# Performance work log

Measured on AMD Instinct MI355X. Metric: run time of the kernel, lower is better.

## Reference

```python
import jax, jax.numpy as jnp
import numpy as np

B, H, S, D = 2, 16, 2048, 64

def setup_inputs() -> dict:
    key = jax.random.key(0)
    kq, kk, kv, km, ks = jax.random.split(key, 5)
    return {
        "query_input": jax.random.normal(kq, (B, H, S, D), dtype=jnp.float32),
        "key_input": jax.random.normal(kk, (B, H, S, D), dtype=jnp.float32),
        "value_input": jax.random.normal(kv, (B, H, S, D), dtype=jnp.float32),
        "query_mask": jnp.ones((B, 1, S, 1), dtype=jnp.float32),
        "key_mask": jax.random.uniform(km, (B, 1, 1, S), dtype=jnp.float32),
        "scale_factor": jax.random.normal(ks, (B, 1, 1, 1), dtype=jnp.float32),
        "dropout": 0,
    }

def reference(query_input, key_input, value_input, query_mask, key_mask, scale_factor, dropout):
    # qk = q @ k^T  -> [B, H, S, S]
    qk = jnp.einsum("bhqd,bhkd->bhqk", query_input, key_input)
    scaled_qk = qk * scale_factor                      # elementwise per-batch scale
    softmax_qk = jax.nn.softmax(scaled_qk, axis=-1)
    masked = softmax_qk * key_mask                     # post-softmax multiplicative mask
    # dropout with p=0 is the identity (deterministic baseline)
    output = jnp.einsum("bhqk,bhkd->bhqd", masked, value_input)
    return output
```

## Files before the change

kernel.cpp:

```cpp
#include <hip/hip_runtime.h>
#include <hip/hip_bf16.h>
#include <stdint.h>

#define BB 2
#define HH 16
#define SS 2048
#define DD 64
constexpr int BH = BB * HH;
constexpr int NT = SS / 64;
constexpr int QB = 16;

typedef _Float16 f16_t;
typedef f16_t f16x8 __attribute__((ext_vector_type(8)));
typedef float f32x4 __attribute__((ext_vector_type(4)));

__device__ __forceinline__ uint32_t pkf16(float a, float b) {
    return __builtin_bit_cast(uint32_t, __builtin_amdgcn_cvt_pkrtz(a, b));
}
__device__ __forceinline__ float fmax3(float a, float b, float c) {
    return fmaxf(fmaxf(a, b), c);
}

__global__ __launch_bounds__(256)
void prepack(const float* __restrict__ Kg, const float* __restrict__ Vg,
             const float* __restrict__ Mg, f16_t* __restrict__ Kp,
             f16_t* __restrict__ Vp)
{
    __shared__ float Vs[64][65];
    const int bh = blockIdx.x % BH;
    const int kt = blockIdx.x / BH;
    const int b  = bh / HH;
    const int t  = threadIdx.x;
    const size_t gbase = (size_t)bh * SS * DD + (size_t)kt * 64 * DD;
    const size_t tbase = ((size_t)bh * NT + kt) * 4096;

    for (int c = t; c < 512; c += 256) {
        const int row = c >> 3, j = c & 7;
        const float* kp = Kg + gbase + (size_t)row * DD + j * 8;
        float4 a = *(const float4*)kp;
        float4 d = *(const float4*)(kp + 4);
        uint4 w = make_uint4(pkf16(a.x, a.y), pkf16(a.z, a.w),
                             pkf16(d.x, d.y), pkf16(d.z, d.w));
        *(uint4*)&Kp[tbase + (size_t)row * 64 + ((j ^ (row & 7)) * 8)] = w;
    }

    for (int c = t; c < 1024; c += 256) {
        const int key = c >> 4, dc = (c & 15) * 4;
        float4 v = *(const float4*)(Vg + gbase + (size_t)key * DD + dc);
        const float m = Mg[(size_t)b * SS + kt * 64 + key];
        Vs[key][dc + 0] = v.x * m;
        Vs[key][dc + 1] = v.y * m;
        Vs[key][dc + 2] = v.z * m;
        Vs[key][dc + 3] = v.w * m;
    }
    __syncthreads();

    for (int c = t; c < 512; c += 256) {
        const int dr = c >> 3, j = c & 7;
        float v0 = Vs[j * 8 + 0][dr], v1 = Vs[j * 8 + 1][dr];
        float v2 = Vs[j * 8 + 2][dr], v3 = Vs[j * 8 + 3][dr];
        float v4 = Vs[j * 8 + 4][dr], v5 = Vs[j * 8 + 5][dr];
        float v6 = Vs[j * 8 + 6][dr], v7 = Vs[j * 8 + 7][dr];
        uint4 w = make_uint4(pkf16(v0, v1), pkf16(v2, v3),
                             pkf16(v4, v5), pkf16(v6, v7));
        *(uint4*)&Vp[tbase + (size_t)dr * 64 + ((j ^ (dr & 7)) * 8)] = w;
    }
}

__global__ __launch_bounds__(512)
void fattn10(const float* __restrict__ Qg, const f16_t* __restrict__ Kp,
             const f16_t* __restrict__ Vp, const float* __restrict__ Sg,
             float* __restrict__ Og)
{
    __shared__ __align__(16) f16_t Kt[2][4096];
    __shared__ __align__(16) f16_t Vt[3][4096];
    __shared__ __align__(16) f16_t Pt[8][16][72];

    const int bh   = blockIdx.x % BH;
    const int qt   = blockIdx.x / BH;
    const int b    = bh / HH;
    const int tid  = threadIdx.x;
    const int wave = tid >> 6;
    const int lane = tid & 63;
    const int l16  = lane & 15;
    const int quad = lane >> 4;

    const float sc = Sg[b] * 1.44269504088896340736f;
    const size_t base = (size_t)bh * SS * DD;
    const size_t tb0  = (size_t)bh * NT * 4096;
    const int q0 = qt * 128 + wave * 16;

    auto stage = [&](int kt, int kbuf, int vbuf) {
        const f16_t* ks = Kp + tb0 + (size_t)kt * 4096 + tid * 8;
        const f16_t* vs = Vp + tb0 + (size_t)kt * 4096 + tid * 8;
        __builtin_amdgcn_global_load_lds(
            (const __attribute__((address_space(1))) void*)ks,
            (__attribute__((address_space(3))) void*)&Kt[kbuf][wave * 512],
            16, 0, 0);
        __builtin_amdgcn_global_load_lds(
            (const __attribute__((address_space(1))) void*)vs,
            (__attribute__((address_space(3))) void*)&Vt[vbuf][wave * 512],
            16, 0, 0);
    };

    stage(0, 0, 0);

    f16x8 qf[2];
    {
        const float* qp = Qg + base + (size_t)(q0 + l16) * DD + quad * 8;
#pragma unroll
        for (int kc = 0; kc < 2; ++kc) {
            float4 a  = *(const float4*)(qp + kc * 32);
            float4 b4 = *(const float4*)(qp + kc * 32 + 4);
            f16x8 f;
            f[0] = (f16_t)(a.x * sc);  f[1] = (f16_t)(a.y * sc);
            f[2] = (f16_t)(a.z * sc);  f[3] = (f16_t)(a.w * sc);
            f[4] = (f16_t)(b4.x * sc); f[5] = (f16_t)(b4.y * sc);
            f[6] = (f16_t)(b4.z * sc); f[7] = (f16_t)(b4.w * sc);
            qf[kc] = f;
        }
    }

    f16x8 ones;
#pragma unroll
    for (int i = 0; i < 8; ++i) ones[i] = (f16_t)1.0f;

    f32x4 Ot[4];
#pragma unroll
    for (int mt = 0; mt < 4; ++mt) Ot[mt] = f32x4{0.f, 0.f, 0.f, 0.f};
    f32x4 Osum = f32x4{0.f, 0.f, 0.f, 0.f};
    float m_run = -1e30f;

    const int swz = (l16 & 7) << 3;

    int vcur = 0;
    for (int kt = 0; kt < NT; ++kt) {
        const int kcur = kt & 1;
        const int vnxt = (vcur == 2) ? 0 : vcur + 1;
        if (kt + 1 < NT) {
            stage(kt + 1, kcur ^ 1, vnxt);
            asm volatile("s_waitcnt vmcnt(2)" ::: "memory");
        } else {
            asm volatile("s_waitcnt vmcnt(0)" ::: "memory");
        }
        __builtin_amdgcn_s_barrier();

        __builtin_amdgcn_s_setprio(1);
        f32x4 Sfr[4];
#pragma unroll
        for (int mt = 0; mt < 4; ++mt) {
            f32x4 acc = f32x4{0.f, 0.f, 0.f, 0.f};
#pragma unroll
            for (int kc = 0; kc < 2; ++kc) {
                const int off = (mt * 16 + l16) * 64 + ((kc * 32 + quad * 8) ^ swz);
                f16x8 kh = *(const f16x8*)&Kt[kcur][off];
                acc = __builtin_amdgcn_mfma_f32_16x16x32_f16(kh, qf[kc], acc, 0, 0, 0);
            }
            Sfr[mt] = acc;
        }

        if (kt > 0) {
            const int vprv = (vcur == 0) ? 2 : vcur - 1;
#pragma unroll
            for (int kc = 0; kc < 2; ++kc) {
                f16x8 pf = *(const f16x8*)&Pt[wave][l16][kc * 32 + quad * 8];
#pragma unroll
                for (int mt = 0; mt < 4; ++mt) {
                    const int off = (mt * 16 + l16) * 64 + ((kc * 32 + quad * 8) ^ swz);
                    f16x8 vf = *(const f16x8*)&Vt[vprv][off];
                    Ot[mt] = __builtin_amdgcn_mfma_f32_16x16x32_f16(vf, pf, Ot[mt], 0, 0, 0);
                }
                Osum = __builtin_amdgcn_mfma_f32_16x16x32_f16(ones, pf, Osum, 0, 0, 0);
            }
        }
        __builtin_amdgcn_s_setprio(0);

        float g0 = fmax3(Sfr[0][0], Sfr[0][1], Sfr[0][2]);
        float g1 = fmax3(Sfr[0][3], Sfr[1][0], Sfr[1][1]);
        float g2 = fmax3(Sfr[1][2], Sfr[1][3], Sfr[2][0]);
        float g3 = fmax3(Sfr[2][1], Sfr[2][2], Sfr[2][3]);
        float g4 = fmax3(Sfr[3][0], Sfr[3][1], Sfr[3][2]);
        float h0 = fmax3(g0, g1, Sfr[3][3]);
        float h1 = fmax3(g2, g3, g4);
        const float lmax = fmaxf(h0, h1);

        if (__any(lmax > m_run + 8.0f)) {
            float mxq = fmaxf(lmax, __shfl_xor(lmax, 16));
            mxq = fmaxf(mxq, __shfl_xor(mxq, 32));
            const float mnew  = fmaxf(m_run, mxq);
            const float alpha = __builtin_amdgcn_exp2f(m_run - mnew);
            m_run = mnew;
#pragma unroll
            for (int mt = 0; mt < 4; ++mt) Ot[mt] *= alpha;
            Osum *= alpha;
        }

        float ps[4][4];
#pragma unroll
        for (int mt = 0; mt < 4; ++mt)
#pragma unroll
            for (int r = 0; r < 4; ++r)
                ps[mt][r] = __builtin_amdgcn_exp2f(Sfr[mt][r] - m_run);

#pragma unroll
        for (int mt = 0; mt < 4; ++mt) {
            uint2 w = make_uint2(pkf16(ps[mt][0], ps[mt][1]),
                                 pkf16(ps[mt][2], ps[mt][3]));
            *(uint2*)&Pt[wave][l16][mt * 16 + quad * 4] = w;
        }

        __builtin_amdgcn_s_barrier();
        vcur = vnxt;
    }

    {
        const int vprv = (vcur == 0) ? 2 : vcur - 1;
#pragma unroll
        for (int kc = 0; kc < 2; ++kc) {
            f16x8 pf = *(const f16x8*)&Pt[wave][l16][kc * 32 + quad * 8];
#pragma unroll
            for (int mt = 0; mt < 4; ++mt) {
                const int off = (mt * 16 + l16) * 64 + ((kc * 32 + quad * 8) ^ swz);
                f16x8 vf = *(const f16x8*)&Vt[vprv][off];
                Ot[mt] = __builtin_amdgcn_mfma_f32_16x16x32_f16(vf, pf, Ot[mt], 0, 0, 0);
            }
            Osum = __builtin_amdgcn_mfma_f32_16x16x32_f16(ones, pf, Osum, 0, 0, 0);
        }
    }

    const float inv = 1.0f / Osum[0];
    float* op = Og + base + (size_t)(q0 + l16) * DD + quad * 4;
#pragma unroll
    for (int mt = 0; mt < 4; ++mt) {
#pragma unroll
        for (int r = 0; r < 4; ++r)
            op[mt * 16 + r] = Ot[mt][r] * inv;
    }
}

__global__ __launch_bounds__(512)
void fattn6(const float* __restrict__ Qg, const float* __restrict__ Kg,
            const float* __restrict__ Vg, const float* __restrict__ Mg,
            const float* __restrict__ Sg, float* __restrict__ Og)
{
    __shared__ __align__(16) f16_t Kh_lds[64][72];
    __shared__ __align__(16) f16_t Vt_lds[64][72];
    __shared__ __align__(16) f16_t Pt_lds[8][16][72];
    __shared__ float msk_lds[SS];

    const int bh   = blockIdx.x % BH;
    const int qt   = blockIdx.x / BH;
    const int b    = bh / HH;
    const int tid  = threadIdx.x;
    const int wave = tid >> 6;
    const int lane = tid & 63;
    const int l16  = lane & 15;
    const int quad = lane >> 4;

    const float sc = Sg[b] * 1.44269504088896340736f;
    const size_t base = (size_t)bh * SS * DD;
    const int q0 = qt * 128 + wave * 16;

    for (int i = tid; i < SS; i += 512) msk_lds[i] = Mg[(size_t)b * SS + i];

    f16x8 qf[2];
    {
        const float* qp = Qg + base + (size_t)(q0 + l16) * DD + quad * 8;
#pragma unroll
        for (int kc = 0; kc < 2; ++kc) {
            float4 a  = *(const float4*)(qp + kc * 32);
            float4 b4 = *(const float4*)(qp + kc * 32 + 4);
            f16x8 f;
            f[0] = (f16_t)(a.x * sc);  f[1] = (f16_t)(a.y * sc);
            f[2] = (f16_t)(a.z * sc);  f[3] = (f16_t)(a.w * sc);
            f[4] = (f16_t)(b4.x * sc); f[5] = (f16_t)(b4.y * sc);
            f[6] = (f16_t)(b4.z * sc); f[7] = (f16_t)(b4.w * sc);
            qf[kc] = f;
        }
    }

    f32x4 Ot[4];
#pragma unroll
    for (int mt = 0; mt < 4; ++mt) Ot[mt] = f32x4{0.f, 0.f, 0.f, 0.f};
    float m_run = -1e30f, l_run = 0.0f;

    const int krow = tid >> 3;
    const int kc8  = (tid & 7) * 8;
    const int vd   = tid & 63;
    const int vk0  = (tid >> 6) * 8;

    for (int kt = 0; kt < NT; ++kt) {
        __syncthreads();
        {
            const float* kp = Kg + base + (size_t)(kt * 64 + krow) * DD + kc8;
            float4 a0 = *(const float4*)(kp);
            float4 a1 = *(const float4*)(kp + 4);
            uint4 w = make_uint4(pkf16(a0.x, a0.y), pkf16(a0.z, a0.w),
                                 pkf16(a1.x, a1.y), pkf16(a1.z, a1.w));
            *(uint4*)&Kh_lds[krow][kc8] = w;
        }
        {
            const float* vp = Vg + base + (size_t)(kt * 64 + vk0) * DD + vd;
            const float* mp = &msk_lds[kt * 64 + vk0];
            float v0 = vp[0 * DD] * mp[0], v1 = vp[1 * DD] * mp[1];
            float v2 = vp[2 * DD] * mp[2], v3 = vp[3 * DD] * mp[3];
            float v4 = vp[4 * DD] * mp[4], v5 = vp[5 * DD] * mp[5];
            float v6 = vp[6 * DD] * mp[6], v7 = vp[7 * DD] * mp[7];
            uint4 w = make_uint4(pkf16(v0, v1), pkf16(v2, v3),
                                 pkf16(v4, v5), pkf16(v6, v7));
            *(uint4*)&Vt_lds[vd][vk0] = w;
        }
        __syncthreads();

        f32x4 Sfr[4];
#pragma unroll
        for (int mt = 0; mt < 4; ++mt) {
            f32x4 acc = f32x4{0.f, 0.f, 0.f, 0.f};
#pragma unroll
            for (int kc = 0; kc < 2; ++kc) {
                f16x8 kh = *(const f16x8*)&Kh_lds[mt * 16 + l16][kc * 32 + quad * 8];
                acc = __builtin_amdgcn_mfma_f32_16x16x32_f16(kh, qf[kc], acc, 0, 0, 0);
            }
            Sfr[mt] = acc;
        }

        float mx = Sfr[0][0];
#pragma unroll
        for (int mt = 0; mt < 4; ++mt)
#pragma unroll
            for (int r = 0; r < 4; ++r) mx = fmaxf(mx, Sfr[mt][r]);
        mx = fmaxf(mx, __shfl_xor(mx, 16));
        mx = fmaxf(mx, __shfl_xor(mx, 32));

        if (__any(mx > m_run)) {
            const float mnew  = fmaxf(m_run, mx);
            const float alpha = exp2f(m_run - mnew);
            m_run = mnew;
            l_run *= alpha;
#pragma unroll
            for (int mt = 0; mt < 4; ++mt) Ot[mt] *= alpha;
        }

        float ps[4][4];
        float rs = 0.0f;
#pragma unroll
        for (int mt = 0; mt < 4; ++mt)
#pragma unroll
            for (int r = 0; r < 4; ++r) {
                ps[mt][r] = exp2f(Sfr[mt][r] - m_run);
                rs += ps[mt][r];
            }
        rs += __shfl_xor(rs, 16);
        rs += __shfl_xor(rs, 32);
        l_run += rs;

#pragma unroll
        for (int mt = 0; mt < 4; ++mt) {
            uint2 w = make_uint2(pkf16(ps[mt][0], ps[mt][1]),
                                 pkf16(ps[mt][2], ps[mt][3]));
            *(uint2*)&Pt_lds[wave][l16][mt * 16 + quad * 4] = w;
        }

#pragma unroll
        for (int kc = 0; kc < 2; ++kc) {
            f16x8 pf = *(const f16x8*)&Pt_lds[wave][l16][kc * 32 + quad * 8];
#pragma unroll
            for (int mt = 0; mt < 4; ++mt) {
                f16x8 vf = *(const f16x8*)&Vt_lds[mt * 16 + l16][kc * 32 + quad * 8];
                Ot[mt] = __builtin_amdgcn_mfma_f32_16x16x32_f16(vf, pf, Ot[mt], 0, 0, 0);
            }
        }
    }

    const float inv = 1.0f / l_run;
    float* op = Og + base + (size_t)(q0 + l16) * DD + quad * 4;
#pragma unroll
    for (int mt = 0; mt < 4; ++mt) {
#pragma unroll
        for (int r = 0; r < 4; ++r)
            op[mt * 16 + r] = Ot[mt][r] * inv;
    }
}

extern "C" void kernel_launch(void* const* d_in, const int* in_sizes, int n_in,
                              void* d_out, int out_size, void* d_ws, size_t ws_size,
                              hipStream_t stream) {
    const float* Qg = (const float*)d_in[0];
    const float* Kg = (const float*)d_in[1];
    const float* Vg = (const float*)d_in[2];
    const float* Mg = (const float*)d_in[4];
    const float* Sg = (const float*)d_in[5];
    float* Og = (float*)d_out;

    const size_t kv_elems = (size_t)BH * SS * DD;
    const size_t need = 2 * kv_elems * sizeof(f16_t);

    if (d_ws != nullptr && ws_size >= need) {
        f16_t* Kp = (f16_t*)d_ws;
        f16_t* Vp = Kp + kv_elems;
        prepack<<<dim3(BH * NT), dim3(256), 0, stream>>>(Kg, Vg, Mg, Kp, Vp);
        fattn10<<<dim3(BH * QB), dim3(512), 0, stream>>>(Qg, Kp, Vp, Sg, Og);
    } else {
        fattn6<<<dim3(BH * QB), dim3(512), 0, stream>>>(Qg, Kg, Vg, Mg, Sg, Og);
    }
}
```

Before: 146.6 us.

## Give each wave two 16-row query groups to reuse K/V fragments

```diff
diff --git a/kernel.cpp b/kernel.cpp
--- a/kernel.cpp
+++ b/kernel.cpp
@@ -67,14 +67,14 @@
     }
 }
 
-__global__ __launch_bounds__(512)
-void fattn10(const float* __restrict__ Qg, const f16_t* __restrict__ Kp,
+__global__ __launch_bounds__(256)
+void fattn12(const float* __restrict__ Qg, const f16_t* __restrict__ Kp,
              const f16_t* __restrict__ Vp, const float* __restrict__ Sg,
              float* __restrict__ Og)
 {
     __shared__ __align__(16) f16_t Kt[2][4096];
     __shared__ __align__(16) f16_t Vt[3][4096];
-    __shared__ __align__(16) f16_t Pt[8][16][72];
+    __shared__ __align__(16) f16_t Pt[4][2][16][72];
 
     const int bh   = blockIdx.x % BH;
     const int qt   = blockIdx.x / BH;
@@ -88,26 +88,36 @@
     const float sc = Sg[b] * 1.44269504088896340736f;
     const size_t base = (size_t)bh * SS * DD;
     const size_t tb0  = (size_t)bh * NT * 4096;
-    const int q0 = qt * 128 + wave * 16;
+    const int q0 = qt * 128 + wave * 32;
 
     auto stage = [&](int kt, int kbuf, int vbuf) {
-        const f16_t* ks = Kp + tb0 + (size_t)kt * 4096 + tid * 8;
-        const f16_t* vs = Vp + tb0 + (size_t)kt * 4096 + tid * 8;
+        const size_t toff = tb0 + (size_t)kt * 4096 + wave * 1024 + lane * 8;
+        const f16_t* ks = Kp + toff;
+        const f16_t* vs = Vp + toff;
         __builtin_amdgcn_global_load_lds(
             (const __attribute__((address_space(1))) void*)ks,
-            (__attribute__((address_space(3))) void*)&Kt[kbuf][wave * 512],
+            (__attribute__((address_space(3))) void*)&Kt[kbuf][wave * 1024],
+            16, 0, 0);
+        __builtin_amdgcn_global_load_lds(
+            (const __attribute__((address_space(1))) void*)(ks + 512),
+            (__attribute__((address_space(3))) void*)&Kt[kbuf][wave * 1024 + 512],
             16, 0, 0);
         __builtin_amdgcn_global_load_lds(
             (const __attribute__((address_space(1))) void*)vs,
-            (__attribute__((address_space(3))) void*)&Vt[vbuf][wave * 512],
+            (__attribute__((address_space(3))) void*)&Vt[vbuf][wave * 1024],
+            16, 0, 0);
+        __builtin_amdgcn_global_load_lds(
+            (const __attribute__((address_space(1))) void*)(vs + 512),
+            (__attribute__((address_space(3))) void*)&Vt[vbuf][wave * 1024 + 512],
             16, 0, 0);
     };
 
     stage(0, 0, 0);
 
-    f16x8 qf[2];
-    {
-        const float* qp = Qg + base + (size_t)(q0 + l16) * DD + quad * 8;
+    f16x8 qf[2][2];
+#pragma unroll
+    for (int g = 0; g < 2; ++g) {
+        const float* qp = Qg + base + (size_t)(q0 + g * 16 + l16) * DD + quad * 8;
 #pragma unroll
         for (int kc = 0; kc < 2; ++kc) {
             float4 a  = *(const float4*)(qp + kc * 32);
@@ -117,7 +127,7 @@
             f[2] = (f16_t)(a.z * sc);  f[3] = (f16_t)(a.w * sc);
             f[4] = (f16_t)(b4.x * sc); f[5] = (f16_t)(b4.y * sc);
             f[6] = (f16_t)(b4.z * sc); f[7] = (f16_t)(b4.w * sc);
-            qf[kc] = f;
+            qf[g][kc] = f;
         }
     }
 
@@ -125,11 +135,13 @@
 #pragma unroll
     for (int i = 0; i < 8; ++i) ones[i] = (f16_t)1.0f;
 
-    f32x4 Ot[4];
-#pragma unroll
-    for (int mt = 0; mt < 4; ++mt) Ot[mt] = f32x4{0.f, 0.f, 0.f, 0.f};
-    f32x4 Osum = f32x4{0.f, 0.f, 0.f, 0.f};
-    float m_run = -1e30f;
+    f32x4 Ot[2][4];
+#pragma unroll
+    for (int g = 0; g < 2; ++g)
+#pragma unroll
+        for (int mt = 0; mt < 4; ++mt) Ot[g][mt] = f32x4{0.f, 0.f, 0.f, 0.f};
+    f32x4 Osum[2] = {f32x4{0.f, 0.f, 0.f, 0.f}, f32x4{0.f, 0.f, 0.f, 0.f}};
+    float m_run[2] = {-1e30f, -1e30f};
 
     const int swz = (l16 & 7) << 3;
 
@@ -139,74 +151,83 @@
         const int vnxt = (vcur == 2) ? 0 : vcur + 1;
         if (kt + 1 < NT) {
             stage(kt + 1, kcur ^ 1, vnxt);
-            asm volatile("s_waitcnt vmcnt(2)" ::: "memory");
+            asm volatile("s_waitcnt vmcnt(4)" ::: "memory");
         } else {
             asm volatile("s_waitcnt vmcnt(0)" ::: "memory");
         }
         __builtin_amdgcn_s_barrier();
 
         __builtin_amdgcn_s_setprio(1);
-        f32x4 Sfr[4];
+        f32x4 Sfr[2][4];
 #pragma unroll
         for (int mt = 0; mt < 4; ++mt) {
-            f32x4 acc = f32x4{0.f, 0.f, 0.f, 0.f};
+            f32x4 a0 = f32x4{0.f, 0.f, 0.f, 0.f};
+            f32x4 a1 = f32x4{0.f, 0.f, 0.f, 0.f};
 #pragma unroll
             for (int kc = 0; kc < 2; ++kc) {
                 const int off = (mt * 16 + l16) * 64 + ((kc * 32 + quad * 8) ^ swz);
                 f16x8 kh = *(const f16x8*)&Kt[kcur][off];
-                acc = __builtin_amdgcn_mfma_f32_16x16x32_f16(kh, qf[kc], acc, 0, 0, 0);
-            }
-            Sfr[mt] = acc;
+                a0 = __builtin_amdgcn_mfma_f32_16x16x32_f16(kh, qf[0][kc], a0, 0, 0, 0);
+                a1 = __builtin_amdgcn_mfma_f32_16x16x32_f16(kh, qf[1][kc], a1, 0, 0, 0);
+            }
+            Sfr[0][mt] = a0;
+            Sfr[1][mt] = a1;
         }
 
         if (kt > 0) {
             const int vprv = (vcur == 0) ? 2 : vcur - 1;
 #pragma unroll
             for (int kc = 0; kc < 2; ++kc) {
-                f16x8 pf = *(const f16x8*)&Pt[wave][l16][kc * 32 + quad * 8];
+                f16x8 pf0 = *(const f16x8*)&Pt[wave][0][l16][kc * 32 + quad * 8];
+                f16x8 pf1 = *(const f16x8*)&Pt[wave][1][l16][kc * 32 + quad * 8];
 #pragma unroll
                 for (int mt = 0; mt < 4; ++mt) {
                     const int off = (mt * 16 + l16) * 64 + ((kc * 32 + quad * 8) ^ swz);
                     f16x8 vf = *(const f16x8*)&Vt[vprv][off];
-                    Ot[mt] = __builtin_amdgcn_mfma_f32_16x16x32_f16(vf, pf, Ot[mt], 0, 0, 0);
+                    Ot[0][mt] = __builtin_amdgcn_mfma_f32_16x16x32_f16(vf, pf0, Ot[0][mt], 0, 0, 0);
+                    Ot[1][mt] = __builtin_amdgcn_mfma_f32_16x16x32_f16(vf, pf1, Ot[1][mt], 0, 0, 0);
                 }
-                Osum = __builtin_amdgcn_mfma_f32_16x16x32_f16(ones, pf, Osum, 0, 0, 0);
+                Osum[0] = __builtin_amdgcn_mfma_f32_16x16x32_f16(ones, pf0, Osum[0], 0, 0, 0);
+                Osum[1] = __builtin_amdgcn_mfma_f32_16x16x32_f16(ones, pf1, Osum[1], 0, 0, 0);
             }
         }
         __builtin_amdgcn_s_setprio(0);
 
-        float g0 = fmax3(Sfr[0][0], Sfr[0][1], Sfr[0][2]);
-        float g1 = fmax3(Sfr[0][3], Sfr[1][0], Sfr[1][1]);
-        float g2 = fmax3(Sfr[1][2], Sfr[1][3], Sfr[2][0]);
-        float g3 = fmax3(Sfr[2][1], Sfr[2][2], Sfr[2][3]);
-        float g4 = fmax3(Sfr[3][0], Sfr[3][1], Sfr[3][2]);
-        float h0 = fmax3(g0, g1, Sfr[3][3]);
-        float h1 = fmax3(g2, g3, g4);
-        const float lmax = fmaxf(h0, h1);
-
-        if (__any(lmax > m_run + 8.0f)) {
-            float mxq = fmaxf(lmax, __shfl_xor(lmax, 16));
-            mxq = fmaxf(mxq, __shfl_xor(mxq, 32));
-            const float mnew  = fmaxf(m_run, mxq);
-            const float alpha = __builtin_amdgcn_exp2f(m_run - mnew);
-            m_run = mnew;
-#pragma unroll
-            for (int mt = 0; mt < 4; ++mt) Ot[mt] *= alpha;
-            Osum *= alpha;
-        }
-
-        float ps[4][4];
-#pragma unroll
-        for (int mt = 0; mt < 4; ++mt)
-#pragma unroll
-            for (int r = 0; r < 4; ++r)
-                ps[mt][r] = __builtin_amdgcn_exp2f(Sfr[mt][r] - m_run);
-
-#pragma unroll
-        for (int mt = 0; mt < 4; ++mt) {
-            uint2 w = make_uint2(pkf16(ps[mt][0], ps[mt][1]),
-                                 pkf16(ps[mt][2], ps[mt][3]));
-            *(uint2*)&Pt[wave][l16][mt * 16 + quad * 4] = w;
+#pragma unroll
+        for (int g = 0; g < 2; ++g) {
+            float g0 = fmax3(Sfr[g][0][0], Sfr[g][0][1], Sfr[g][0][2]);
+            float g1 = fmax3(Sfr[g][0][3], Sfr[g][1][0], Sfr[g][1][1]);
+            float g2 = fmax3(Sfr[g][1][2], Sfr[g][1][3], Sfr[g][2][0]);
+            float g3 = fmax3(Sfr[g][2][1], Sfr[g][2][2], Sfr[g][2][3]);
+            float g4 = fmax3(Sfr[g][3][0], Sfr[g][3][1], Sfr[g][3][2]);
+            float h0 = fmax3(g0, g1, Sfr[g][3][3]);
+            float h1 = fmax3(g2, g3, g4);
+            const float lmax = fmaxf(h0, h1);
+
+            if (__any(lmax > m_run[g] + 8.0f)) {
+                float mxq = fmaxf(lmax, __shfl_xor(lmax, 16));
+                mxq = fmaxf(mxq, __shfl_xor(mxq, 32));
+                const float mnew  = fmaxf(m_run[g], mxq);
+                const float alpha = __builtin_amdgcn_exp2f(m_run[g] - mnew);
+                m_run[g] = mnew;
+#pragma unroll
+                for (int mt = 0; mt < 4; ++mt) Ot[g][mt] *= alpha;
+                Osum[g] *= alpha;
+            }
+
+            float ps[4][4];
+#pragma unroll
+            for (int mt = 0; mt < 4; ++mt)
+#pragma unroll
+                for (int r = 0; r < 4; ++r)
+                    ps[mt][r] = __builtin_amdgcn_exp2f(Sfr[g][mt][r] - m_run[g]);
+
+#pragma unroll
+            for (int mt = 0; mt < 4; ++mt) {
+                uint2 w = make_uint2(pkf16(ps[mt][0], ps[mt][1]),
+                                     pkf16(ps[mt][2], ps[mt][3]));
+                *(uint2*)&Pt[wave][g][l16][mt * 16 + quad * 4] = w;
+            }
         }
 
         __builtin_amdgcn_s_barrier();
@@ -217,24 +238,30 @@
         const int vprv = (vcur == 0) ? 2 : vcur - 1;
 #pragma unroll
         for (int kc = 0; kc < 2; ++kc) {
-            f16x8 pf = *(const f16x8*)&Pt[wave][l16][kc * 32 + quad * 8];
+            f16x8 pf0 = *(const f16x8*)&Pt[wave][0][l16][kc * 32 + quad * 8];
+            f16x8 pf1 = *(const f16x8*)&Pt[wave][1][l16][kc * 32 + quad * 8];
 #pragma unroll
             for (int mt = 0; mt < 4; ++mt) {
                 const int off = (mt * 16 + l16) * 64 + ((kc * 32 + quad * 8) ^ swz);
                 f16x8 vf = *(const f16x8*)&Vt[vprv][off];
-                Ot[mt] = __builtin_amdgcn_mfma_f32_16x16x32_f16(vf, pf, Ot[mt], 0, 0, 0);
-            }
-            Osum = __builtin_amdgcn_mfma_f32_16x16x32_f16(ones, pf, Osum, 0, 0, 0);
-        }
-    }
-
-    const float inv = 1.0f / Osum[0];
-    float* op = Og + base + (size_t)(q0 + l16) * DD + quad * 4;
-#pragma unroll
-    for (int mt = 0; mt < 4; ++mt) {
-#pragma unroll
-        for (int r = 0; r < 4; ++r)
-            op[mt * 16 + r] = Ot[mt][r] * inv;
+                Ot[0][mt] = __builtin_amdgcn_mfma_f32_16x16x32_f16(vf, pf0, Ot[0][mt], 0, 0, 0);
+                Ot[1][mt] = __builtin_amdgcn_mfma_f32_16x16x32_f16(vf, pf1, Ot[1][mt], 0, 0, 0);
+            }
+            Osum[0] = __builtin_amdgcn_mfma_f32_16x16x32_f16(ones, pf0, Osum[0], 0, 0, 0);
+            Osum[1] = __builtin_amdgcn_mfma_f32_16x16x32_f16(ones, pf1, Osum[1], 0, 0, 0);
+        }
+    }
+
+#pragma unroll
+    for (int g = 0; g < 2; ++g) {
+        const float inv = 1.0f / Osum[g][0];
+        float* op = Og + base + (size_t)(q0 + g * 16 + l16) * DD + quad * 4;
+#pragma unroll
+        for (int mt = 0; mt < 4; ++mt) {
+#pragma unroll
+            for (int r = 0; r < 4; ++r)
+                op[mt * 16 + r] = Ot[g][mt][r] * inv;
+        }
     }
 }
 
@@ -399,7 +426,7 @@
         f16_t* Kp = (f16_t*)d_ws;
         f16_t* Vp = Kp + kv_elems;
         prepack<<<dim3(BH * NT), dim3(256), 0, stream>>>(Kg, Vg, Mg, Kp, Vp);
-        fattn10<<<dim3(BH * QB), dim3(512), 0, stream>>>(Qg, Kp, Vp, Sg, Og);
+        fattn12<<<dim3(BH * QB), dim3(256), 0, stream>>>(Qg, Kp, Vp, Sg, Og);
     } else {
         fattn6<<<dim3(BH * QB), dim3(512), 0, stream>>>(Qg, Kg, Vg, Mg, Sg, Og);
     }
```

Measured after the change: 158.0 us. +7.7%, slower.

## Stagger K and V prefetch with double buffers and unroll loop by two

Applied to the files above, without the earlier changes.

```diff
diff --git a/kernel.cpp b/kernel.cpp
--- a/kernel.cpp
+++ b/kernel.cpp
@@ -68,12 +68,12 @@
 }
 
 __global__ __launch_bounds__(512)
-void fattn10(const float* __restrict__ Qg, const f16_t* __restrict__ Kp,
+void fattn13(const float* __restrict__ Qg, const f16_t* __restrict__ Kp,
              const f16_t* __restrict__ Vp, const float* __restrict__ Sg,
              float* __restrict__ Og)
 {
     __shared__ __align__(16) f16_t Kt[2][4096];
-    __shared__ __align__(16) f16_t Vt[3][4096];
+    __shared__ __align__(16) f16_t Vt[2][4096];
     __shared__ __align__(16) f16_t Pt[8][16][72];
 
     const int bh   = blockIdx.x % BH;
@@ -90,20 +90,21 @@
     const size_t tb0  = (size_t)bh * NT * 4096;
     const int q0 = qt * 128 + wave * 16;
 
-    auto stage = [&](int kt, int kbuf, int vbuf) {
-        const f16_t* ks = Kp + tb0 + (size_t)kt * 4096 + tid * 8;
-        const f16_t* vs = Vp + tb0 + (size_t)kt * 4096 + tid * 8;
+    const f16_t* kroot = Kp + tb0 + tid * 8;
+    const f16_t* vroot = Vp + tb0 + tid * 8;
+
+    auto stageK = [&](int t, int buf) {
         __builtin_amdgcn_global_load_lds(
-            (const __attribute__((address_space(1))) void*)ks,
-            (__attribute__((address_space(3))) void*)&Kt[kbuf][wave * 512],
-            16, 0, 0);
+            (const __attribute__((address_space(1))) void*)(kroot + (size_t)t * 4096),
+            (__attribute__((address_space(3))) void*)&Kt[buf][wave * 512], 16, 0, 0);
+    };
+    auto stageV = [&](int t, int buf) {
         __builtin_amdgcn_global_load_lds(
-            (const __attribute__((address_space(1))) void*)vs,
-            (__attribute__((address_space(3))) void*)&Vt[vbuf][wave * 512],
-            16, 0, 0);
+            (const __attribute__((address_space(1))) void*)(vroot + (size_t)t * 4096),
+            (__attribute__((address_space(3))) void*)&Vt[buf][wave * 512], 16, 0, 0);
     };
 
-    stage(0, 0, 0);
+    stageK(0, 0);
 
     f16x8 qf[2];
     {
@@ -133,16 +134,11 @@
 
     const int swz = (l16 & 7) << 3;
 
-    int vcur = 0;
-    for (int kt = 0; kt < NT; ++kt) {
-        const int kcur = kt & 1;
-        const int vnxt = (vcur == 2) ? 0 : vcur + 1;
-        if (kt + 1 < NT) {
-            stage(kt + 1, kcur ^ 1, vnxt);
-            asm volatile("s_waitcnt vmcnt(2)" ::: "memory");
-        } else {
-            asm volatile("s_waitcnt vmcnt(0)" ::: "memory");
-        }
+    auto phase = [&](int t, int ksb, int vsb, int krb, int vrb, bool doPV) {
+        const int tk = (t + 1 < NT) ? (t + 1) : (NT - 1);
+        stageK(tk, ksb);
+        stageV(t, vsb);
+        asm volatile("s_waitcnt vmcnt(2)" ::: "memory");
         __builtin_amdgcn_s_barrier();
 
         __builtin_amdgcn_s_setprio(1);
@@ -153,21 +149,20 @@
 #pragma unroll
             for (int kc = 0; kc < 2; ++kc) {
                 const int off = (mt * 16 + l16) * 64 + ((kc * 32 + quad * 8) ^ swz);
-                f16x8 kh = *(const f16x8*)&Kt[kcur][off];
+                f16x8 kh = *(const f16x8*)&Kt[krb][off];
                 acc = __builtin_amdgcn_mfma_f32_16x16x32_f16(kh, qf[kc], acc, 0, 0, 0);
             }
             Sfr[mt] = acc;
         }
 
-        if (kt > 0) {
-            const int vprv = (vcur == 0) ? 2 : vcur - 1;
+        if (doPV) {
 #pragma unroll
             for (int kc = 0; kc < 2; ++kc) {
                 f16x8 pf = *(const f16x8*)&Pt[wave][l16][kc * 32 + quad * 8];
 #pragma unroll
                 for (int mt = 0; mt < 4; ++mt) {
                     const int off = (mt * 16 + l16) * 64 + ((kc * 32 + quad * 8) ^ swz);
-                    f16x8 vf = *(const f16x8*)&Vt[vprv][off];
+                    f16x8 vf = *(const f16x8*)&Vt[vrb][off];
                     Ot[mt] = __builtin_amdgcn_mfma_f32_16x16x32_f16(vf, pf, Ot[mt], 0, 0, 0);
                 }
                 Osum = __builtin_amdgcn_mfma_f32_16x16x32_f16(ones, pf, Osum, 0, 0, 0);
@@ -210,18 +205,25 @@
         }
 
         __builtin_amdgcn_s_barrier();
-        vcur = vnxt;
-    }
-
+    };
+
+    phase(0, 1, 0, 0, 1, false);
+    phase(1, 0, 1, 1, 0, true);
+    for (int j = 1; j < NT / 2; ++j) {
+        phase(2 * j,     1, 0, 0, 1, true);
+        phase(2 * j + 1, 0, 1, 1, 0, true);
+    }
+
+    asm volatile("s_waitcnt vmcnt(0)" ::: "memory");
+    __builtin_amdgcn_s_barrier();
     {
-        const int vprv = (vcur == 0) ? 2 : vcur - 1;
 #pragma unroll
         for (int kc = 0; kc < 2; ++kc) {
             f16x8 pf = *(const f16x8*)&Pt[wave][l16][kc * 32 + quad * 8];
 #pragma unroll
             for (int mt = 0; mt < 4; ++mt) {
                 const int off = (mt * 16 + l16) * 64 + ((kc * 32 + quad * 8) ^ swz);
-                f16x8 vf = *(const f16x8*)&Vt[vprv][off];
+                f16x8 vf = *(const f16x8*)&Vt[1][off];
                 Ot[mt] = __builtin_amdgcn_mfma_f32_16x16x32_f16(vf, pf, Ot[mt], 0, 0, 0);
             }
             Osum = __builtin_amdgcn_mfma_f32_16x16x32_f16(ones, pf, Osum, 0, 0, 0);
@@ -399,7 +401,7 @@
         f16_t* Kp = (f16_t*)d_ws;
         f16_t* Vp = Kp + kv_elems;
         prepack<<<dim3(BH * NT), dim3(256), 0, stream>>>(Kg, Vg, Mg, Kp, Vp);
-        fattn10<<<dim3(BH * QB), dim3(512), 0, stream>>>(Qg, Kp, Vp, Sg, Og);
+        fattn13<<<dim3(BH * QB), dim3(512), 0, stream>>>(Qg, Kp, Vp, Sg, Og);
     } else {
         fattn6<<<dim3(BH * QB), dim3(512), 0, stream>>>(Qg, Kg, Vg, Mg, Sg, Og);
     }
```

Result: no change. 145.4 us, median of 2 (-0.9%).
